# Performance work log

Measured on AMD Instinct MI355X. Metric: run time of the kernel, lower is better.

## Reference

```python
import jax, jax.numpy as jnp
import numpy as np

NUM_BINS = 20
TEMPERATURE = 0.1
EPS = 1e-8


def setup_inputs() -> dict:
    key = jax.random.key(0)
    k1, k2 = jax.random.split(key)
    shape = (32, 1, 1024, 1024)  # B, C, H, W segmentation-style probability maps
    preds = jax.random.uniform(k1, shape, dtype=jnp.float32)
    targets = jax.random.uniform(k2, shape, dtype=jnp.float32)
    return {"preds": preds, "targets": targets}


def reference(preds, targets):
    p = preds.reshape(-1)
    t = targets.reshape(-1)
    centers = jnp.linspace(0.0, 1.0, NUM_BINS, dtype=p.dtype)

    def per_bin(c):
        # Gaussian soft-assignment weights for this bin center
        w = jnp.exp(-(p - c) ** 2 / TEMPERATURE)
        w_sum = w.sum()
        e = (w * p).sum() / (w_sum + EPS)  # weighted mean confidence
        o = (w * t).sum() / (w_sum + EPS)  # weighted mean accuracy
        # torch code skips bins with zero total weight
        return jnp.where(w_sum == 0.0, jnp.zeros_like(e), jnp.abs(e - o))

    # lax.map loops sequentially over the 20 bin centers so we never
    # materialize a [NUM_BINS, N] weight matrix.
    contribs = jax.lax.map(per_bin, centers)
    return contribs.sum() / NUM_BINS
```

## Files before the change

kernel.cpp:

```cpp
#include <hip/hip_runtime.h>
#include <math.h>

#define NUM_BINS 20
#define NPAIR    (NUM_BINS / 2)
#define NACC     (3 * NUM_BINS)
#define BLOCK    256
#define NBLK     1024

typedef float v2f __attribute__((ext_vector_type(2)));

__device__ __host__ constexpr float K1f() { return (float)(-1.0 / (0.1 * 0.6931471805599453)); }
__device__ __host__ constexpr float K2f() { return (float)( 2.0 / (1.9 * 0.6931471805599453)); }

__global__ __launch_bounds__(BLOCK, 4) void ace_partial(const float* __restrict__ p,
                                                        const float* __restrict__ t,
                                                        float* __restrict__ partials,
                                                        int n4, int nblk) {
    const float K1 = K1f();
    const float K2 = K2f();

    v2f aW2[NPAIR], aP2[NPAIR], aT2[NPAIR];
#pragma unroll
    for (int jp = 0; jp < NPAIR; ++jp) {
        aW2[jp] = (v2f){0.f, 0.f};
        aP2[jp] = (v2f){0.f, 0.f};
        aT2[jp] = (v2f){0.f, 0.f};
    }

    const float4* __restrict__ p4 = (const float4*)p;
    const float4* __restrict__ t4 = (const float4*)t;

    int tid    = blockIdx.x * BLOCK + threadIdx.x;
    int stride = gridDim.x * BLOCK;

    int i = tid;
    if (i < n4) {
        float4 pv = p4[i];
        float4 tv = t4[i];
        for (;;) {
            int inext = i + stride;
            bool more = (inext < n4);
            float4 pvn, tvn;
            if (more) { pvn = p4[inext]; tvn = t4[inext]; }

            float pe[4] = {pv.x, pv.y, pv.z, pv.w};
            float te[4] = {tv.x, tv.y, tv.z, tv.w};

#pragma unroll
            for (int e = 0; e < 4; ++e) {
                float pp = pe[e];
                float tt = te[e];
                float u  = __builtin_amdgcn_exp2f(K1 * pp * pp);
                float G  = __builtin_amdgcn_exp2f(K2 * pp);
                float GG = G * G;
                v2f g2;  g2.x = u;  g2.y = u * G;
                v2f GG2 = (v2f){GG, GG};
                v2f pp2 = (v2f){pp, pp};
                v2f tt2 = (v2f){tt, tt};
#pragma unroll
                for (int jp = 0; jp < NPAIR; ++jp) {
                    aW2[jp] += g2;
                    aP2[jp]  = __builtin_elementwise_fma(g2, pp2, aP2[jp]);
                    aT2[jp]  = __builtin_elementwise_fma(g2, tt2, aT2[jp]);
                    g2      *= GG2;
                }
            }

            if (!more) break;
            pv = pvn; tv = tvn; i = inext;
        }
    }

#pragma unroll
    for (int jp = 0; jp < NPAIR; ++jp) {
#pragma unroll
        for (int off = 32; off > 0; off >>= 1) {
            aW2[jp].x += __shfl_down(aW2[jp].x, off, 64);
            aW2[jp].y += __shfl_down(aW2[jp].y, off, 64);
            aP2[jp].x += __shfl_down(aP2[jp].x, off, 64);
            aP2[jp].y += __shfl_down(aP2[jp].y, off, 64);
            aT2[jp].x += __shfl_down(aT2[jp].x, off, 64);
            aT2[jp].y += __shfl_down(aT2[jp].y, off, 64);
        }
    }

    __shared__ float red[BLOCK / 64][NACC];
    int wave = threadIdx.x >> 6;
    int lane = threadIdx.x & 63;
    if (lane == 0) {
#pragma unroll
        for (int jp = 0; jp < NPAIR; ++jp) {
            red[wave][2 * jp]                    = aW2[jp].x;
            red[wave][2 * jp + 1]                = aW2[jp].y;
            red[wave][NUM_BINS + 2 * jp]         = aP2[jp].x;
            red[wave][NUM_BINS + 2 * jp + 1]     = aP2[jp].y;
            red[wave][2 * NUM_BINS + 2 * jp]     = aT2[jp].x;
            red[wave][2 * NUM_BINS + 2 * jp + 1] = aT2[jp].y;
        }
    }
    __syncthreads();

    if (threadIdx.x < NACC) {
        float s = 0.f;
#pragma unroll
        for (int w = 0; w < BLOCK / 64; ++w) s += red[w][threadIdx.x];
        partials[threadIdx.x * nblk + blockIdx.x] = s;
    }
}

__global__ __launch_bounds__(1024) void ace_final(const float* __restrict__ partials,
                                                  float* __restrict__ out,
                                                  int nblk) {
    const float K1 = K1f();

    __shared__ float red[NACC][16];
    __shared__ float sums[NACC];
    int tid = threadIdx.x;

    if (tid < NACC * 16) {
        int j = tid >> 4;
        int k = tid & 15;
        float s = 0.f;
        for (int b = k; b < nblk; b += 16) s += partials[j * nblk + b];
        red[j][k] = s;
    }
    __syncthreads();

    if (tid < NACC) {
        float s = 0.f;
#pragma unroll
        for (int k = 0; k < 16; ++k) s += red[tid][k];
        sums[tid] = s;
    }
    __syncthreads();

    if (tid == 0) {
        float acc = 0.f;
        for (int j = 0; j < NUM_BINS; ++j) {
            float c    = (float)j / 19.0f;
            float A    = __builtin_amdgcn_exp2f(K1 * c * c);
            float wsum = A * sums[j];
            float denom = wsum + 1e-8f;
            float e    = (A * sums[NUM_BINS + j]) / denom;
            float o    = (A * sums[2 * NUM_BINS + j]) / denom;
            float contrib = (wsum == 0.0f) ? 0.0f : fabsf(e - o);
            acc += contrib;
        }
        out[0] = acc / (float)NUM_BINS;
    }
}

extern "C" void kernel_launch(void* const* d_in, const int* in_sizes, int n_in,
                              void* d_out, int out_size, void* d_ws, size_t ws_size,
                              hipStream_t stream) {
    const float* preds   = (const float*)d_in[0];
    const float* targets = (const float*)d_in[1];
    float* out           = (float*)d_out;
    float* partials      = (float*)d_ws;

    int n  = in_sizes[0];
    int n4 = n >> 2;

    int nblk = NBLK;
    size_t need = (size_t)nblk * NACC * sizeof(float);
    if (ws_size < need) {
        nblk = (int)(ws_size / (NACC * sizeof(float)));
        if (nblk < 1) nblk = 1;
    }

    ace_partial<<<nblk, BLOCK, 0, stream>>>(preds, targets, partials, n4, nblk);
    ace_final<<<1, 1024, 0, stream>>>(partials, out, nblk);
}
```

Before: 300.8 us.

## Stage input tiles through LDS with async global_load_lds double buffering

Replaces the register-prefetched grid-stride loop with a double-buffered LDS pipeline that uses global_load_lds to copy the next tile of preds and targets while the current tile is processed. It aims to hide memory latency without holding prefetch registers. In exchange it adds a block-wide barrier every iteration, LDS traffic, and a scalar tail loop. The loop appears compute-bound on the 20-bin accumulation, so the gain may be limited.

```diff
diff --git a/kernel.cpp b/kernel.cpp
--- a/kernel.cpp
+++ b/kernel.cpp
@@ -1,21 +1,32 @@
 #include <hip/hip_runtime.h>
 #include <math.h>
+#include <stdint.h>
 
 #define NUM_BINS 20
 #define NPAIR    (NUM_BINS / 2)
 #define NACC     (3 * NUM_BINS)
 #define BLOCK    256
 #define NBLK     1024
+#define TILEF    (BLOCK * 4)
 
 typedef float v2f __attribute__((ext_vector_type(2)));
+typedef __attribute__((address_space(3))) uint32_t       lds_u32_t;
+typedef __attribute__((address_space(1))) const uint32_t glb_u32_t;
 
 __device__ __host__ constexpr float K1f() { return (float)(-1.0 / (0.1 * 0.6931471805599453)); }
 __device__ __host__ constexpr float K2f() { return (float)( 2.0 / (1.9 * 0.6931471805599453)); }
+
+__device__ __forceinline__ void stage16(const float4* gsrc, float* ldst) {
+    __builtin_amdgcn_global_load_lds((glb_u32_t*)gsrc, (lds_u32_t*)ldst, 16, 0, 0);
+}
 
 __global__ __launch_bounds__(BLOCK, 4) void ace_partial(const float* __restrict__ p,
                                                         const float* __restrict__ t,
                                                         float* __restrict__ partials,
                                                         int n4, int nblk) {
+    __shared__ float ldsP[2][TILEF];
+    __shared__ float ldsT[2][TILEF];
+
     const float K1 = K1f();
     const float K2 = K2f();
 
@@ -30,44 +41,86 @@
     const float4* __restrict__ p4 = (const float4*)p;
     const float4* __restrict__ t4 = (const float4*)t;
 
-    int tid    = blockIdx.x * BLOCK + threadIdx.x;
-    int stride = gridDim.x * BLOCK;
-
-    int i = tid;
-    if (i < n4) {
+    const int tid    = threadIdx.x;
+    const int wave   = tid >> 6;
+    const int stride = gridDim.x * BLOCK;
+    int gidx         = blockIdx.x * BLOCK + tid;
+    const int niter  = n4 / stride;
+
+    float* const ldsPbase = &ldsP[0][0];
+    float* const ldsTbase = &ldsT[0][0];
+    const int waveOff = wave * 256;
+
+    int cur = 0;
+    if (niter > 0) {
+        stage16(p4 + gidx, ldsPbase + waveOff);
+        stage16(t4 + gidx, ldsTbase + waveOff);
+        asm volatile("s_waitcnt vmcnt(0)" ::: "memory");
+        __syncthreads();
+    }
+
+    for (int k = 0; k < niter; ++k) {
+        const int gnext = gidx + stride;
+        if (k + 1 < niter) {
+            const int nb = cur ^ 1;
+            stage16(p4 + gnext, ldsPbase + nb * TILEF + waveOff);
+            stage16(t4 + gnext, ldsTbase + nb * TILEF + waveOff);
+        }
+
+        const float4 pv = *(const float4*)(ldsPbase + cur * TILEF + tid * 4);
+        const float4 tv = *(const float4*)(ldsTbase + cur * TILEF + tid * 4);
+
+        float pe[4] = {pv.x, pv.y, pv.z, pv.w};
+        float te[4] = {tv.x, tv.y, tv.z, tv.w};
+
+#pragma unroll
+        for (int e = 0; e < 4; ++e) {
+            float pp = pe[e];
+            float tt = te[e];
+            float u  = __builtin_amdgcn_exp2f(K1 * pp * pp);
+            float G  = __builtin_amdgcn_exp2f(K2 * pp);
+            float GG = G * G;
+            v2f g2;  g2.x = u;  g2.y = u * G;
+            v2f GG2 = (v2f){GG, GG};
+            v2f pp2 = (v2f){pp, pp};
+            v2f tt2 = (v2f){tt, tt};
+#pragma unroll
+            for (int jp = 0; jp < NPAIR; ++jp) {
+                aW2[jp] += g2;
+                aP2[jp]  = __builtin_elementwise_fma(g2, pp2, aP2[jp]);
+                aT2[jp]  = __builtin_elementwise_fma(g2, tt2, aT2[jp]);
+                g2      *= GG2;
+            }
+        }
+
+        __syncthreads();
+        cur ^= 1;
+        gidx = gnext;
+    }
+
+    for (int i = gidx; i < n4; i += stride) {
         float4 pv = p4[i];
         float4 tv = t4[i];
-        for (;;) {
-            int inext = i + stride;
-            bool more = (inext < n4);
-            float4 pvn, tvn;
-            if (more) { pvn = p4[inext]; tvn = t4[inext]; }
-
-            float pe[4] = {pv.x, pv.y, pv.z, pv.w};
-            float te[4] = {tv.x, tv.y, tv.z, tv.w};
-
-#pragma unroll
-            for (int e = 0; e < 4; ++e) {
-                float pp = pe[e];
-                float tt = te[e];
-                float u  = __builtin_amdgcn_exp2f(K1 * pp * pp);
-                float G  = __builtin_amdgcn_exp2f(K2 * pp);
-                float GG = G * G;
-                v2f g2;  g2.x = u;  g2.y = u * G;
-                v2f GG2 = (v2f){GG, GG};
-                v2f pp2 = (v2f){pp, pp};
-                v2f tt2 = (v2f){tt, tt};
-#pragma unroll
-                for (int jp = 0; jp < NPAIR; ++jp) {
-                    aW2[jp] += g2;
-                    aP2[jp]  = __builtin_elementwise_fma(g2, pp2, aP2[jp]);
-                    aT2[jp]  = __builtin_elementwise_fma(g2, tt2, aT2[jp]);
-                    g2      *= GG2;
-                }
+        float pe[4] = {pv.x, pv.y, pv.z, pv.w};
+        float te[4] = {tv.x, tv.y, tv.z, tv.w};
+#pragma unroll
+        for (int e = 0; e < 4; ++e) {
+            float pp = pe[e];
+            float tt = te[e];
+            float u  = __builtin_amdgcn_exp2f(K1 * pp * pp);
+            float G  = __builtin_amdgcn_exp2f(K2 * pp);
+            float GG = G * G;
+            v2f g2;  g2.x = u;  g2.y = u * G;
+            v2f GG2 = (v2f){GG, GG};
+            v2f pp2 = (v2f){pp, pp};
+            v2f tt2 = (v2f){tt, tt};
+#pragma unroll
+            for (int jp = 0; jp < NPAIR; ++jp) {
+                aW2[jp] += g2;
+                aP2[jp]  = __builtin_elementwise_fma(g2, pp2, aP2[jp]);
+                aT2[jp]  = __builtin_elementwise_fma(g2, tt2, aT2[jp]);
+                g2      *= GG2;
             }
-
-            if (!more) break;
-            pv = pvn; tv = tvn; i = inext;
         }
     }
 
@@ -85,7 +138,6 @@
     }
 
     __shared__ float red[BLOCK / 64][NACC];
-    int wave = threadIdx.x >> 6;
     int lane = threadIdx.x & 63;
     if (lane == 0) {
 #pragma unroll
```

Measured after the change: 301.9 us. About the same (+0.4%).

## Raise occupancy: float2 loads, no prefetch, more blocks, vectorized final reduce

Applied to the files above, without the earlier changes.

The partial kernel now loads float2 instead of float4 and drops the manual next-iteration prefetch. Together with launch bounds raised from 4 to 6 blocks per CU and the grid grown from 1024 to 1536 blocks, this is meant to cut register pressure and let more waves hide latency in this compute-bound loop. The final kernel reads partials as float4. The trade-off is fewer loads in flight per thread and possible spills under the tighter register budget.

```diff
diff --git a/kernel.cpp b/kernel.cpp
--- a/kernel.cpp
+++ b/kernel.cpp
@@ -5,17 +5,17 @@
 #define NPAIR    (NUM_BINS / 2)
 #define NACC     (3 * NUM_BINS)
 #define BLOCK    256
-#define NBLK     1024
+#define NBLK     1536
 
 typedef float v2f __attribute__((ext_vector_type(2)));
 
 __device__ __host__ constexpr float K1f() { return (float)(-1.0 / (0.1 * 0.6931471805599453)); }
 __device__ __host__ constexpr float K2f() { return (float)( 2.0 / (1.9 * 0.6931471805599453)); }
 
-__global__ __launch_bounds__(BLOCK, 4) void ace_partial(const float* __restrict__ p,
+__global__ __launch_bounds__(BLOCK, 6) void ace_partial(const float* __restrict__ p,
                                                         const float* __restrict__ t,
                                                         float* __restrict__ partials,
-                                                        int n4, int nblk) {
+                                                        int n2, int nblk) {
     const float K1 = K1f();
     const float K2 = K2f();
 
@@ -27,47 +27,32 @@
         aT2[jp] = (v2f){0.f, 0.f};
     }
 
-    const float4* __restrict__ p4 = (const float4*)p;
-    const float4* __restrict__ t4 = (const float4*)t;
+    const float2* __restrict__ p2 = (const float2*)p;
+    const float2* __restrict__ t2 = (const float2*)t;
 
-    int tid    = blockIdx.x * BLOCK + threadIdx.x;
-    int stride = gridDim.x * BLOCK;
-
-    int i = tid;
-    if (i < n4) {
-        float4 pv = p4[i];
-        float4 tv = t4[i];
-        for (;;) {
-            int inext = i + stride;
-            bool more = (inext < n4);
-            float4 pvn, tvn;
-            if (more) { pvn = p4[inext]; tvn = t4[inext]; }
-
-            float pe[4] = {pv.x, pv.y, pv.z, pv.w};
-            float te[4] = {tv.x, tv.y, tv.z, tv.w};
+    const int stride = gridDim.x * BLOCK;
+    for (int i = blockIdx.x * BLOCK + threadIdx.x; i < n2; i += stride) {
+        const float2 pv = p2[i];
+        const float2 tv = t2[i];
 
 #pragma unroll
-            for (int e = 0; e < 4; ++e) {
-                float pp = pe[e];
-                float tt = te[e];
-                float u  = __builtin_amdgcn_exp2f(K1 * pp * pp);
-                float G  = __builtin_amdgcn_exp2f(K2 * pp);
-                float GG = G * G;
-                v2f g2;  g2.x = u;  g2.y = u * G;
-                v2f GG2 = (v2f){GG, GG};
-                v2f pp2 = (v2f){pp, pp};
-                v2f tt2 = (v2f){tt, tt};
+        for (int e = 0; e < 2; ++e) {
+            const float pp = (e == 0) ? pv.x : pv.y;
+            const float tt = (e == 0) ? tv.x : tv.y;
+            float u  = __builtin_amdgcn_exp2f(K1 * pp * pp);
+            float G  = __builtin_amdgcn_exp2f(K2 * pp);
+            float GG = G * G;
+            v2f g2;  g2.x = u;  g2.y = u * G;
+            const v2f GG2 = (v2f){GG, GG};
+            const v2f pp2 = (v2f){pp, pp};
+            const v2f tt2 = (v2f){tt, tt};
 #pragma unroll
-                for (int jp = 0; jp < NPAIR; ++jp) {
-                    aW2[jp] += g2;
-                    aP2[jp]  = __builtin_elementwise_fma(g2, pp2, aP2[jp]);
-                    aT2[jp]  = __builtin_elementwise_fma(g2, tt2, aT2[jp]);
-                    g2      *= GG2;
-                }
+            for (int jp = 0; jp < NPAIR; ++jp) {
+                aW2[jp] += g2;
+                aP2[jp]  = __builtin_elementwise_fma(g2, pp2, aP2[jp]);
+                aT2[jp]  = __builtin_elementwise_fma(g2, tt2, aT2[jp]);
+                g2      *= GG2;
             }
-
-            if (!more) break;
-            pv = pvn; tv = tvn; i = inext;
         }
     }
 
@@ -85,8 +70,8 @@
     }
 
     __shared__ float red[BLOCK / 64][NACC];
-    int wave = threadIdx.x >> 6;
-    int lane = threadIdx.x & 63;
+    const int wave = threadIdx.x >> 6;
+    const int lane = threadIdx.x & 63;
     if (lane == 0) {
 #pragma unroll
         for (int jp = 0; jp < NPAIR; ++jp) {
@@ -120,8 +105,14 @@
     if (tid < NACC * 16) {
         int j = tid >> 4;
         int k = tid & 15;
+        const float4* row4 = (const float4*)(partials + (size_t)j * nblk);
+        int n4b = nblk >> 2;
         float s = 0.f;
-        for (int b = k; b < nblk; b += 16) s += partials[j * nblk + b];
+        for (int b = k; b < n4b; b += 16) {
+            float4 v = row4[b];
+            s += (v.x + v.y) + (v.z + v.w);
+        }
+        for (int b = (n4b << 2) + k; b < nblk; b += 16) s += partials[(size_t)j * nblk + b];
         red[j][k] = s;
     }
     __syncthreads();
@@ -159,7 +150,7 @@
     float* partials      = (float*)d_ws;
 
     int n  = in_sizes[0];
-    int n4 = n >> 2;
+    int n2 = n >> 1;
 
     int nblk = NBLK;
     size_t need = (size_t)nblk * NACC * sizeof(float);
@@ -168,6 +159,6 @@
         if (nblk < 1) nblk = 1;
     }
 
-    ace_partial<<<nblk, BLOCK, 0, stream>>>(preds, targets, partials, n4, nblk);
+    ace_partial<<<nblk, BLOCK, 0, stream>>>(preds, targets, partials, n2, nblk);
     ace_final<<<1, 1024, 0, stream>>>(partials, out, nblk);
 }
```

Result: slower. 312.2 us (+3.8%).
